# Optimization experiments

Hardware: AMD Instinct MI355X
Metric: run time of the kernel (lower is better)

Reference implementation:

```python
import jax, jax.numpy as jnp
import numpy as np

NUM_STREAM = 4
SINKHORN_ITERS = 20
HC_EPS = 1e-06
NORM_EPS = 1e-06


def sinkhorn_knopps(h, iters, eps):
    # h: [B, S, ns, ns]
    h = jax.nn.softmax(h, axis=-1) + eps
    h = h / (h.sum(-2, keepdims=True) + eps)
    for _ in range(iters - 1):  # fixed small trip count (19), unrolled
        h = h / (h.sum(-1, keepdims=True) + eps)
        h = h / (h.sum(-2, keepdims=True) + eps)
    return h


def setup_inputs() -> dict:
    key = jax.random.key(0)
    k1, k2, k3, k4 = jax.random.split(key, 4)
    B, S, ns, H = 4, 2048, NUM_STREAM, 1024
    mix_hc = (2 + ns) * ns  # 24
    x = jax.random.normal(k1, (B, S, ns, H), dtype=jnp.float32)
    hc_fn = jax.random.normal(k2, (mix_hc, ns * H), dtype=jnp.float32) * 0.02
    hc_scale = jax.random.uniform(k3, (3,), dtype=jnp.float32)
    hc_base = jax.random.normal(k4, (mix_hc,), dtype=jnp.float32)
    return {"x": x, "hc_fn": hc_fn, "hc_scale": hc_scale, "hc_base": hc_base}


def reference(x, hc_fn, hc_scale, hc_base):
    B, S, ns, H = x.shape
    xf = x.reshape(B, S, ns * H).astype(jnp.float32)
    # RMSNorm stats (applied as a post-scale on the linear output, as in source)
    rsqrt = jax.lax.rsqrt(jnp.mean(jnp.square(xf), axis=-1, keepdims=True) + NORM_EPS)
    weight = jnp.einsum('bsd,md->bsm', xf, hc_fn) * rsqrt  # [B, S, mix_hc]
    h_pre = weight[..., :ns]
    h_post = weight[..., ns:2 * ns]
    h_res = weight[..., 2 * ns:].reshape(B, S, ns, ns)
    h_pre = jax.nn.sigmoid(h_pre * hc_scale[0] + hc_base[:ns][None, None, :]) + HC_EPS
    h_post = 2.0 * jax.nn.sigmoid(h_post * hc_scale[1] + hc_base[ns:2 * ns][None, None, :])
    h_res = h_res * hc_scale[2] + hc_base[2 * ns:].reshape(ns, ns)[None, None, :, :]
    h_res = sinkhorn_knopps(h_res, SINKHORN_ITERS, HC_EPS)
    xs = xf.reshape(B, S, ns, H)
    # hc_pre: mix streams into a single vector per token
    y = jnp.einsum('bsn,bsnh->bsh', h_pre, xs)  # [B, S, H]
    # hc_post: broadcast gated y back to streams + Sinkhorn-mixed residual streams
    out = h_post[..., None] * y[:, :, None, :] + jnp.einsum('bsij,bsih->bsjh', h_res, xs)
    return out.astype(x.dtype)
```

## Files before the change

kernel.cpp:

```cpp
#include <hip/hip_runtime.h>
#include <math.h>

#define NS 4
#define HDIM 1024
#define DDIM 4096
#define MDIM 24
#define T 4
#define NTH 512
#define HC_EPS_F 1e-6f
#define NORM_EPS_F 1e-6f

__device__ __forceinline__ void gload_lds16(const float* g, float* l) {
  __builtin_amdgcn_global_load_lds(
      (const __attribute__((address_space(1))) void*)g,
      (__attribute__((address_space(3))) void*)l, 16, 0, 0);
}
__device__ __forceinline__ float frcp(float v) { return __builtin_amdgcn_rcpf(v); }

__launch_bounds__(NTH, 4)
__global__ void mhc_fused(const float* __restrict__ x,
                          const float* __restrict__ hc_fn,
                          const float* __restrict__ hc_scale,
                          const float* __restrict__ hc_base,
                          float* __restrict__ out) {
  __shared__ float xs[T * DDIM];
  __shared__ float w_s[MDIM][T];
  __shared__ float ss_s[T];
  __shared__ float hpre_s[T][NS];
  __shared__ float hpost_s[T][NS];
  __shared__ float hres_s[T][NS][NS];

  const int tid  = threadIdx.x;
  const int lane = tid & 63;
  const int wave = tid >> 6;
  const long long tok0 = (long long)blockIdx.x * T;
  const float* xg = x + tok0 * DDIM;

  #pragma unroll
  for (int c = 0; c < 8; ++c)
    gload_lds16(xg + (c * NTH + tid) * 4, xs + (c * NTH + wave * 64) * 4);

  const int mb = wave * 3;
  const float4* fn4[3];
  #pragma unroll
  for (int m = 0; m < 3; ++m)
    fn4[m] = (const float4*)(hc_fn + (long long)(mb + m) * DDIM);
  float4 c_fn[3];
  #pragma unroll
  for (int m = 0; m < 3; ++m) c_fn[m] = fn4[m][lane];

  __syncthreads();

  float acc[3][T];
  float ssq[T];
  #pragma unroll
  for (int m = 0; m < 3; ++m)
    #pragma unroll
    for (int tt = 0; tt < T; ++tt) acc[m][tt] = 0.f;
  #pragma unroll
  for (int tt = 0; tt < T; ++tt) ssq[tt] = 0.f;

  const float4* xs4 = (const float4*)xs;
  #pragma unroll 4
  for (int it = 0; it < 16; ++it) {
    float4 n_fn[3];
    if (it < 15) {
      const int nfl = (it + 1) * 64 + lane;
      #pragma unroll
      for (int m = 0; m < 3; ++m) n_fn[m] = fn4[m][nfl];
    }
    const int fl = it * 64 + lane;
    #pragma unroll
    for (int tt = 0; tt < T; ++tt) {
      const float4 xv = xs4[tt * 1024 + fl];
      if (wave == 7)
        ssq[tt] = fmaf(xv.x, xv.x, fmaf(xv.y, xv.y, fmaf(xv.z, xv.z, fmaf(xv.w, xv.w, ssq[tt]))));
      #pragma unroll
      for (int m = 0; m < 3; ++m)
        acc[m][tt] = fmaf(xv.x, c_fn[m].x,
                     fmaf(xv.y, c_fn[m].y,
                     fmaf(xv.z, c_fn[m].z,
                     fmaf(xv.w, c_fn[m].w, acc[m][tt]))));
    }
    #pragma unroll
    for (int m = 0; m < 3; ++m) c_fn[m] = n_fn[m];
  }

  #pragma unroll
  for (int m = 0; m < 3; ++m)
    #pragma unroll
    for (int tt = 0; tt < T; ++tt) {
      float v = acc[m][tt];
      #pragma unroll
      for (int off = 32; off > 0; off >>= 1) v += __shfl_xor(v, off, 64);
      if (lane == 0) w_s[mb + m][tt] = v;
    }
  if (wave == 7) {
    #pragma unroll
    for (int tt = 0; tt < T; ++tt) {
      float v = ssq[tt];
      #pragma unroll
      for (int off = 32; off > 0; off >>= 1) v += __shfl_xor(v, off, 64);
      if (lane == 0) ss_s[tt] = v;
    }
  }
  __syncthreads();

  if (wave < T) {
    const int tt = wave;
    const int e  = lane & 15;
    const float rs = rsqrtf(ss_s[tt] * (1.0f / DDIM) + NORM_EPS_F);
    const float s0 = hc_scale[0], s1 = hc_scale[1], s2 = hc_scale[2];

    float h = w_s[8 + e][tt] * rs * s2 + hc_base[8 + e];
    float mx = fmaxf(h, __shfl_xor(h, 1, 4));
    mx = fmaxf(mx, __shfl_xor(mx, 2, 4));
    float ex = expf(h - mx);
    float sm = ex + __shfl_xor(ex, 1, 4);
    sm += __shfl_xor(sm, 2, 4);
    h = ex * frcp(sm) + HC_EPS_F;
    float cs = h + __shfl_xor(h, 4, 16);
    cs += __shfl_xor(cs, 8, 16);
    h *= frcp(cs + HC_EPS_F);
    #pragma unroll 1
    for (int itn = 0; itn < 19; ++itn) {
      float rsum = h + __shfl_xor(h, 1, 4);
      rsum += __shfl_xor(rsum, 2, 4);
      h *= frcp(rsum + HC_EPS_F);
      float csum = h + __shfl_xor(h, 4, 16);
      csum += __shfl_xor(csum, 8, 16);
      h *= frcp(csum + HC_EPS_F);
    }
    if (lane < 16) hres_s[tt][e >> 2][e & 3] = h;
    if (lane < NS) {
      const float wp = w_s[lane][tt] * rs;
      hpre_s[tt][lane] = frcp(1.0f + expf(-(wp * s0 + hc_base[lane]))) + HC_EPS_F;
      const float wq = w_s[NS + lane][tt] * rs;
      hpost_s[tt][lane] = 2.0f * frcp(1.0f + expf(-(wq * s1 + hc_base[NS + lane])));
    }
  }
  __syncthreads();

  {
    const int tt = wave & 3;
    const int hf = wave >> 2;
    float hp[NS], hq[NS], hr[NS][NS];
    #pragma unroll
    for (int i = 0; i < NS; ++i) {
      hp[i] = hpre_s[tt][i];
      hq[i] = hpost_s[tt][i];
      #pragma unroll
      for (int j = 0; j < NS; ++j) hr[i][j] = hres_s[tt][i][j];
    }
    float4* ob = (float4*)(out + (tok0 + tt) * NS * HDIM);
    #pragma unroll
    for (int c = 0; c < 2; ++c) {
      const int h4 = hf * 128 + c * 64 + lane;
      float4 xv[NS];
      #pragma unroll
      for (int i = 0; i < NS; ++i) xv[i] = xs4[tt * 1024 + i * 256 + h4];
      float4 y;
      y.x = hp[0]*xv[0].x + hp[1]*xv[1].x + hp[2]*xv[2].x + hp[3]*xv[3].x;
      y.y = hp[0]*xv[0].y + hp[1]*xv[1].y + hp[2]*xv[2].y + hp[3]*xv[3].y;
      y.z = hp[0]*xv[0].z + hp[1]*xv[1].z + hp[2]*xv[2].z + hp[3]*xv[3].z;
      y.w = hp[0]*xv[0].w + hp[1]*xv[1].w + hp[2]*xv[2].w + hp[3]*xv[3].w;
      #pragma unroll
      for (int n = 0; n < NS; ++n) {
        float4 o;
        o.x = hq[n]*y.x + hr[0][n]*xv[0].x + hr[1][n]*xv[1].x + hr[2][n]*xv[2].x + hr[3][n]*xv[3].x;
        o.y = hq[n]*y.y + hr[0][n]*xv[0].y + hr[1][n]*xv[1].y + hr[2][n]*xv[2].y + hr[3][n]*xv[3].y;
        o.z = hq[n]*y.z + hr[0][n]*xv[0].z + hr[1][n]*xv[1].z + hr[2][n]*xv[2].z + hr[3][n]*xv[3].z;
        o.w = hq[n]*y.w + hr[0][n]*xv[0].w + hr[1][n]*xv[1].w + hr[2][n]*xv[2].w + hr[3][n]*xv[3].w;
        ob[n * 256 + h4] = o;
      }
    }
  }
}

extern "C" void kernel_launch(void* const* d_in, const int* in_sizes, int n_in,
                              void* d_out, int out_size, void* d_ws, size_t ws_size,
                              hipStream_t stream) {
  const float* x        = (const float*)d_in[0];
  const float* hc_fn    = (const float*)d_in[1];
  const float* hc_scale = (const float*)d_in[2];
  const float* hc_base  = (const float*)d_in[3];
  float* out = (float*)d_out;

  const int ntok = in_sizes[0] / DDIM;
  const int grid = ntok / T;
  mhc_fused<<<grid, NTH, 0, stream>>>(x, hc_fn, hc_scale, hc_base, out);
}
```

Before: 112.8 us.

## Split fused kernel into gate-computation and output kernels via workspace

Replaces the single fused kernel with two launches. The first computes the 24 gate values per token over 8-token blocks with double-buffered LDS streaming of x, and writes them to workspace. The second rereads x per token to apply the mix. The aim is smaller LDS footprint and higher occupancy, at the cost of reading x twice from global memory and adding an extra launch.

```diff
diff --git a/kernel.cpp b/kernel.cpp
--- a/kernel.cpp
+++ b/kernel.cpp
@@ -4,9 +4,7 @@
 #define NS 4
 #define HDIM 1024
 #define DDIM 4096
-#define MDIM 24
-#define T 4
-#define NTH 512
+#define T1 8
 #define HC_EPS_F 1e-6f
 #define NORM_EPS_F 1e-6f
 
@@ -17,99 +15,99 @@
 }
 __device__ __forceinline__ float frcp(float v) { return __builtin_amdgcn_rcpf(v); }
 
-__launch_bounds__(NTH, 4)
-__global__ void mhc_fused(const float* __restrict__ x,
-                          const float* __restrict__ hc_fn,
-                          const float* __restrict__ hc_scale,
-                          const float* __restrict__ hc_base,
-                          float* __restrict__ out) {
-  __shared__ float xs[T * DDIM];
-  __shared__ float w_s[MDIM][T];
-  __shared__ float ss_s[T];
-  __shared__ float hpre_s[T][NS];
-  __shared__ float hpost_s[T][NS];
-  __shared__ float hres_s[T][NS][NS];
+__launch_bounds__(256, 3)
+__global__ void mhc_weights(const float* __restrict__ x,
+                            const float* __restrict__ hc_fn,
+                            const float* __restrict__ hc_scale,
+                            const float* __restrict__ hc_base,
+                            float* __restrict__ gates) {
+  __shared__ float xs[2][T1][256];
+  __shared__ float w_s[25][T1];
 
   const int tid  = threadIdx.x;
   const int lane = tid & 63;
   const int wave = tid >> 6;
-  const long long tok0 = (long long)blockIdx.x * T;
-  const float* xg = x + tok0 * DDIM;
+  const long long tok0 = (long long)blockIdx.x * T1;
+  const float* xg  = x + tok0 * DDIM;
+  const float* xw0 = xg + (2 * wave) * DDIM;
+  const float* xw1 = xg + (2 * wave + 1) * DDIM;
 
+  gload_lds16(xw0 + lane * 4, &xs[0][2 * wave][0]);
+  gload_lds16(xw1 + lane * 4, &xs[0][2 * wave + 1][0]);
+
+  const int mb = wave * 6;
+  const float4* fn4[6];
   #pragma unroll
-  for (int c = 0; c < 8; ++c)
-    gload_lds16(xg + (c * NTH + tid) * 4, xs + (c * NTH + wave * 64) * 4);
+  for (int m = 0; m < 6; ++m)
+    fn4[m] = (const float4*)(hc_fn + (long long)(mb + m) * DDIM);
+  float4 c_fn[6];
+  #pragma unroll
+  for (int m = 0; m < 6; ++m) c_fn[m] = fn4[m][lane];
 
-  const int mb = wave * 3;
-  const float4* fn4[3];
+  float acc[6][T1];
+  float ssq[T1];
   #pragma unroll
-  for (int m = 0; m < 3; ++m)
-    fn4[m] = (const float4*)(hc_fn + (long long)(mb + m) * DDIM);
-  float4 c_fn[3];
+  for (int m = 0; m < 6; ++m)
+    #pragma unroll
+    for (int tt = 0; tt < T1; ++tt) acc[m][tt] = 0.f;
   #pragma unroll
-  for (int m = 0; m < 3; ++m) c_fn[m] = fn4[m][lane];
+  for (int tt = 0; tt < T1; ++tt) ssq[tt] = 0.f;
 
   __syncthreads();
 
-  float acc[3][T];
-  float ssq[T];
-  #pragma unroll
-  for (int m = 0; m < 3; ++m)
-    #pragma unroll
-    for (int tt = 0; tt < T; ++tt) acc[m][tt] = 0.f;
-  #pragma unroll
-  for (int tt = 0; tt < T; ++tt) ssq[tt] = 0.f;
-
-  const float4* xs4 = (const float4*)xs;
-  #pragma unroll 4
+  int buf = 0;
   for (int it = 0; it < 16; ++it) {
-    float4 n_fn[3];
+    float4 n_fn[6];
     if (it < 15) {
+      const int off = (it + 1) * 256 + lane * 4;
+      gload_lds16(xw0 + off, &xs[buf ^ 1][2 * wave][0]);
+      gload_lds16(xw1 + off, &xs[buf ^ 1][2 * wave + 1][0]);
       const int nfl = (it + 1) * 64 + lane;
       #pragma unroll
-      for (int m = 0; m < 3; ++m) n_fn[m] = fn4[m][nfl];
+      for (int m = 0; m < 6; ++m) n_fn[m] = fn4[m][nfl];
     }
-    const int fl = it * 64 + lane;
     #pragma unroll
-    for (int tt = 0; tt < T; ++tt) {
-      const float4 xv = xs4[tt * 1024 + fl];
-      if (wave == 7)
+    for (int tt = 0; tt < T1; ++tt) {
+      const float4 xv = ((const float4*)xs[buf][tt])[lane];
+      if (wave == 3)
         ssq[tt] = fmaf(xv.x, xv.x, fmaf(xv.y, xv.y, fmaf(xv.z, xv.z, fmaf(xv.w, xv.w, ssq[tt]))));
       #pragma unroll
-      for (int m = 0; m < 3; ++m)
+      for (int m = 0; m < 6; ++m)
         acc[m][tt] = fmaf(xv.x, c_fn[m].x,
                      fmaf(xv.y, c_fn[m].y,
                      fmaf(xv.z, c_fn[m].z,
                      fmaf(xv.w, c_fn[m].w, acc[m][tt]))));
     }
     #pragma unroll
-    for (int m = 0; m < 3; ++m) c_fn[m] = n_fn[m];
+    for (int m = 0; m < 6; ++m) c_fn[m] = n_fn[m];
+    __syncthreads();
+    buf ^= 1;
   }
 
   #pragma unroll
-  for (int m = 0; m < 3; ++m)
+  for (int m = 0; m < 6; ++m)
     #pragma unroll
-    for (int tt = 0; tt < T; ++tt) {
+    for (int tt = 0; tt < T1; ++tt) {
       float v = acc[m][tt];
       #pragma unroll
       for (int off = 32; off > 0; off >>= 1) v += __shfl_xor(v, off, 64);
       if (lane == 0) w_s[mb + m][tt] = v;
     }
-  if (wave == 7) {
+  if (wave == 3) {
     #pragma unroll
-    for (int tt = 0; tt < T; ++tt) {
+    for (int tt = 0; tt < T1; ++tt) {
       float v = ssq[tt];
       #pragma unroll
       for (int off = 32; off > 0; off >>= 1) v += __shfl_xor(v, off, 64);
-      if (lane == 0) ss_s[tt] = v;
+      if (lane == 0) w_s[24][tt] = v;
     }
   }
   __syncthreads();
 
-  if (wave < T) {
-    const int tt = wave;
+  if (wave < 2) {
+    const int tt = wave * 4 + (lane >> 4);
     const int e  = lane & 15;
-    const float rs = rsqrtf(ss_s[tt] * (1.0f / DDIM) + NORM_EPS_F);
+    const float rs = rsqrtf(w_s[24][tt] * (1.0f / DDIM) + NORM_EPS_F);
     const float s0 = hc_scale[0], s1 = hc_scale[1], s2 = hc_scale[2];
 
     float h = w_s[8 + e][tt] * rs * s2 + hc_base[8 + e];
@@ -131,49 +129,54 @@
       csum += __shfl_xor(csum, 8, 16);
       h *= frcp(csum + HC_EPS_F);
     }
-    if (lane < 16) hres_s[tt][e >> 2][e & 3] = h;
-    if (lane < NS) {
-      const float wp = w_s[lane][tt] * rs;
-      hpre_s[tt][lane] = frcp(1.0f + expf(-(wp * s0 + hc_base[lane]))) + HC_EPS_F;
-      const float wq = w_s[NS + lane][tt] * rs;
-      hpost_s[tt][lane] = 2.0f * frcp(1.0f + expf(-(wq * s1 + hc_base[NS + lane])));
+    float* g = gates + (tok0 + tt) * 24;
+    g[8 + e] = h;
+    if (e < NS) {
+      const float wp = w_s[e][tt] * rs;
+      g[e] = frcp(1.0f + expf(-(wp * s0 + hc_base[e]))) + HC_EPS_F;
+      const float wq = w_s[NS + e][tt] * rs;
+      g[NS + e] = 2.0f * frcp(1.0f + expf(-(wq * s1 + hc_base[NS + e])));
     }
   }
-  __syncthreads();
+}
 
-  {
-    const int tt = wave & 3;
-    const int hf = wave >> 2;
-    float hp[NS], hq[NS], hr[NS][NS];
+__launch_bounds__(256, 8)
+__global__ void mhc_out(const float* __restrict__ x,
+                        const float* __restrict__ gates,
+                        float* __restrict__ out) {
+  const long long token = blockIdx.x;
+  const int q = threadIdx.x;
+
+  const float* g = gates + token * 24;
+  float hp[NS], hq[NS], hr[NS][NS];
+  #pragma unroll
+  for (int i = 0; i < NS; ++i) {
+    hp[i] = g[i];
+    hq[i] = g[NS + i];
     #pragma unroll
-    for (int i = 0; i < NS; ++i) {
-      hp[i] = hpre_s[tt][i];
-      hq[i] = hpost_s[tt][i];
-      #pragma unroll
-      for (int j = 0; j < NS; ++j) hr[i][j] = hres_s[tt][i][j];
-    }
-    float4* ob = (float4*)(out + (tok0 + tt) * NS * HDIM);
-    #pragma unroll
-    for (int c = 0; c < 2; ++c) {
-      const int h4 = hf * 128 + c * 64 + lane;
-      float4 xv[NS];
-      #pragma unroll
-      for (int i = 0; i < NS; ++i) xv[i] = xs4[tt * 1024 + i * 256 + h4];
-      float4 y;
-      y.x = hp[0]*xv[0].x + hp[1]*xv[1].x + hp[2]*xv[2].x + hp[3]*xv[3].x;
-      y.y = hp[0]*xv[0].y + hp[1]*xv[1].y + hp[2]*xv[2].y + hp[3]*xv[3].y;
-      y.z = hp[0]*xv[0].z + hp[1]*xv[1].z + hp[2]*xv[2].z + hp[3]*xv[3].z;
-      y.w = hp[0]*xv[0].w + hp[1]*xv[1].w + hp[2]*xv[2].w + hp[3]*xv[3].w;
-      #pragma unroll
-      for (int n = 0; n < NS; ++n) {
-        float4 o;
-        o.x = hq[n]*y.x + hr[0][n]*xv[0].x + hr[1][n]*xv[1].x + hr[2][n]*xv[2].x + hr[3][n]*xv[3].x;
-        o.y = hq[n]*y.y + hr[0][n]*xv[0].y + hr[1][n]*xv[1].y + hr[2][n]*xv[2].y + hr[3][n]*xv[3].y;
-        o.z = hq[n]*y.z + hr[0][n]*xv[0].z + hr[1][n]*xv[1].z + hr[2][n]*xv[2].z + hr[3][n]*xv[3].z;
-        o.w = hq[n]*y.w + hr[0][n]*xv[0].w + hr[1][n]*xv[1].w + hr[2][n]*xv[2].w + hr[3][n]*xv[3].w;
-        ob[n * 256 + h4] = o;
-      }
-    }
+    for (int j = 0; j < NS; ++j) hr[i][j] = g[8 + i * NS + j];
+  }
+
+  const float4* xb = (const float4*)(x + token * DDIM);
+  float4 xv[NS];
+  #pragma unroll
+  for (int i = 0; i < NS; ++i) xv[i] = xb[i * 256 + q];
+
+  float4 y;
+  y.x = hp[0]*xv[0].x + hp[1]*xv[1].x + hp[2]*xv[2].x + hp[3]*xv[3].x;
+  y.y = hp[0]*xv[0].y + hp[1]*xv[1].y + hp[2]*xv[2].y + hp[3]*xv[3].y;
+  y.z = hp[0]*xv[0].z + hp[1]*xv[1].z + hp[2]*xv[2].z + hp[3]*xv[3].z;
+  y.w = hp[0]*xv[0].w + hp[1]*xv[1].w + hp[2]*xv[2].w + hp[3]*xv[3].w;
+
+  float4* ob = (float4*)(out + token * DDIM);
+  #pragma unroll
+  for (int n = 0; n < NS; ++n) {
+    float4 o;
+    o.x = hq[n]*y.x + hr[0][n]*xv[0].x + hr[1][n]*xv[1].x + hr[2][n]*xv[2].x + hr[3][n]*xv[3].x;
+    o.y = hq[n]*y.y + hr[0][n]*xv[0].y + hr[1][n]*xv[1].y + hr[2][n]*xv[2].y + hr[3][n]*xv[3].y;
+    o.z = hq[n]*y.z + hr[0][n]*xv[0].z + hr[1][n]*xv[1].z + hr[2][n]*xv[2].z + hr[3][n]*xv[3].z;
+    o.w = hq[n]*y.w + hr[0][n]*xv[0].w + hr[1][n]*xv[1].w + hr[2][n]*xv[2].w + hr[3][n]*xv[3].w;
+    ob[n * 256 + q] = o;
   }
 }
 
@@ -184,9 +187,10 @@
   const float* hc_fn    = (const float*)d_in[1];
   const float* hc_scale = (const float*)d_in[2];
   const float* hc_base  = (const float*)d_in[3];
-  float* out = (float*)d_out;
+  float* out   = (float*)d_out;
+  float* gates = (float*)d_ws;
 
   const int ntok = in_sizes[0] / DDIM;
-  const int grid = ntok / T;
-  mhc_fused<<<grid, NTH, 0, stream>>>(x, hc_fn, hc_scale, hc_base, out);
+  mhc_weights<<<ntok / T1, 256, 0, stream>>>(x, hc_fn, hc_scale, hc_base, gates);
+  mhc_out<<<ntok, 256, 0, stream>>>(x, gates, out);
 }
```

New measurement: 112.1 us. About the same (-0.6%).
